# Kernel optimization log

Measured on AMD Instinct MI355X. Metric: run time of the kernel, lower is better.

The kernel has to match this reference:

```python
import jax, jax.numpy as jnp
import numpy as np

K_SIZE = 5


def extract_patches(x, k):
    # tf.image.extract_patches with SAME padding, stride 1, rate 1.
    # x: (B, H, W, C) -> (B, H, W, k*k, C), patch index ordered row-major (ki, kj),
    # channels last within each tap, matching TF's depth ordering + reshape.
    B, H, W, C = x.shape
    p = k // 2
    xp = jnp.pad(x, ((0, 0), (p, p), (p, p), (0, 0)))
    views = [xp[:, i:i + H, j:j + W, :] for i in range(k) for j in range(k)]
    return jnp.stack(views, axis=3)


def setup_inputs() -> dict:
    key = jax.random.key(0)
    k1, k2, k3, k4 = jax.random.split(key, 4)
    B, H, W, C = 4, 64, 64, 128
    bin_size = 128
    return {
        "main": jax.random.normal(k1, (B, H, W, C), dtype=jnp.float32),
        "main_value": jax.random.normal(k2, (B, H, W, bin_size), dtype=jnp.float32),
        "ref": jax.random.normal(k3, (B, H, W, C), dtype=jnp.float32),
        "ref_value": jax.random.normal(k4, (B, H, W, bin_size), dtype=jnp.float32),
    }


def reference(main, main_value, ref, ref_value):
    # mode == 'dot'
    k = K_SIZE
    main5 = main[:, :, :, None, :]                 # (B,H,W,1,C)
    main_value5 = main_value[:, :, :, None, :]     # (B,H,W,1,bin)
    ref_stacked = extract_patches(ref, k)          # (B,H,W,k*k,C)
    ref_value_stacked = extract_patches(ref_value, k)  # (B,H,W,k*k,bin)
    # concat the center query itself as an extra key/value slot
    ref_con = jnp.concatenate([ref_stacked, main5], axis=3)        # (B,H,W,k*k+1,C)
    attn = jnp.sum(ref_con * main5, axis=4)                         # (B,H,W,k*k+1)
    attn = jax.nn.softmax(attn, axis=3)
    val_con = jnp.concatenate([ref_value_stacked, main_value5], axis=3)  # (B,H,W,k*k+1,bin)
    out = jnp.sum(attn[..., None] * val_con, axis=3)                # (B,H,W,bin)
    return out
```

## Files before the change

kernel.cpp:

```cpp
#include <hip/hip_runtime.h>
#include <math.h>

typedef _Float16 v8h __attribute__((ext_vector_type(8)));
typedef float    v4f __attribute__((ext_vector_type(4)));

#define B_OFF   0
#define ALO_OFF 32768
#define L_OFF   40960
#define P_OFF   57344

__device__ __forceinline__ int swz(int r, int c16) {
    return (r << 8) + ((c16 ^ (r & 15)) << 4);
}

__global__ __launch_bounds__(512, 4) void local_attn_mfma(
    const float* __restrict__ main_,
    const float* __restrict__ main_value,
    const float* __restrict__ ref,
    const float* __restrict__ ref_value,
    float* __restrict__ out)
{
    __shared__ __align__(16) char S[65536];

    const int tid = threadIdx.x;
    const int bid = blockIdx.x;
    const int b  = bid >> 7;
    const int h0 = ((bid >> 3) & 15) << 2;
    const int w0 = (bid & 7) << 3;

    {
        const int r = tid >> 2;
        const int q = tid & 3;
        const float* src;
        bool valid = true;
        if (r < 96) {
            const int hy = r / 12, hx = r - hy * 12;
            const int gh = h0 - 2 + hy, gw = w0 - 2 + hx;
            valid = (gh >= 0) & (gh < 64) & (gw >= 0) & (gw < 64);
            src = ref + (size_t)((((b << 6) + (valid ? gh : 0)) << 6) + (valid ? gw : 0)) * 128;
        } else {
            const int t = r - 96;
            src = main_ + (size_t)((((b << 6) + h0 + (t >> 3)) << 6) + (w0 + (t & 7))) * 128;
        }
        #pragma unroll
        for (int g = 0; g < 4; ++g) {
            const int cbase = (q << 5) + (g << 3);
            float a8[8];
            const float4 v0 = valid ? *(const float4*)(src + cbase)     : make_float4(0,0,0,0);
            const float4 v1 = valid ? *(const float4*)(src + cbase + 4) : make_float4(0,0,0,0);
            a8[0]=v0.x; a8[1]=v0.y; a8[2]=v0.z; a8[3]=v0.w;
            a8[4]=v1.x; a8[5]=v1.y; a8[6]=v1.z; a8[7]=v1.w;
            v8h hi;
            #pragma unroll
            for (int j = 0; j < 8; ++j) hi[j] = (_Float16)a8[j];
            *(v8h*)(S + B_OFF + swz(r, (q << 2) + g)) = hi;
            if (r >= 96) {
                v8h lo;
                #pragma unroll
                for (int j = 0; j < 8; ++j) lo[j] = (_Float16)(a8[j] - (float)hi[j]);
                *(v8h*)(S + ALO_OFF + swz(r - 96, (q << 2) + g)) = lo;
            }
        }
        *(uint4*)(S + P_OFF + tid * 16) = make_uint4(0, 0, 0, 0);
    }
    __syncthreads();

    const int lane = tid & 63, w = tid >> 6;
    const int l15 = lane & 15, quad = lane >> 4;
    const int mt  = w >> 2;
    const int ntp = (w & 3) << 1;

    {
        const int arow = 96 + (mt << 4) + l15;
        const int lrow = (mt << 4) + l15;
        const int b0r  = (ntp << 4) + l15, b1r = b0r + 16;
        v4f acc0 = {0,0,0,0}, acc1 = {0,0,0,0};
        #pragma unroll
        for (int ks = 0; ks < 4; ++ks) {
            const int c16 = (ks << 2) + quad;
            const v8h ahi = *(const v8h*)(S + B_OFF   + swz(arow, c16));
            const v8h alo = *(const v8h*)(S + ALO_OFF + swz(lrow, c16));
            const v8h bb0 = *(const v8h*)(S + B_OFF   + swz(b0r,  c16));
            const v8h bb1 = *(const v8h*)(S + B_OFF   + swz(b1r,  c16));
            acc0 = __builtin_amdgcn_mfma_f32_16x16x32_f16(ahi, bb0, acc0, 0, 0, 0);
            acc0 = __builtin_amdgcn_mfma_f32_16x16x32_f16(alo, bb0, acc0, 0, 0, 0);
            acc1 = __builtin_amdgcn_mfma_f32_16x16x32_f16(ahi, bb1, acc1, 0, 0, 0);
            acc1 = __builtin_amdgcn_mfma_f32_16x16x32_f16(alo, bb1, acc1, 0, 0, 0);
        }
        #pragma unroll
        for (int j = 0; j < 4; ++j) {
            const int px = (mt << 4) + (quad << 2) + j;
            *(float*)(S + L_OFF + (px << 9) + ((((ntp    ) << 4) + l15) << 2)) = acc0[j];
            *(float*)(S + L_OFF + (px << 9) + ((((ntp + 1) << 4) + l15) << 2)) = acc1[j];
        }
    }
    __syncthreads();

    {
        #pragma unroll
        for (int i = 0; i < 4; ++i) {
            const int tk = w + (i << 3);
            const int pb = tk & 15;
            const int ch = ((tk >> 4) << 6) + lane;
            v8h hv;
            #pragma unroll
            for (int j = 0; j < 8; ++j) {
                const int pos = (pb << 3) + j;
                float v;
                if (pos < 96) {
                    const int hy = pos / 12, hx = pos - hy * 12;
                    const int gh = h0 - 2 + hy, gw = w0 - 2 + hx;
                    const bool ok = (gh >= 0) & (gh < 64) & (gw >= 0) & (gw < 64);
                    v = ok ? ref_value[(size_t)((((b << 6) + gh) << 6) + gw) * 128 + ch] : 0.f;
                } else {
                    const int t2 = pos - 96;
                    v = main_value[(size_t)((((b << 6) + h0 + (t2 >> 3)) << 6) + (w0 + (t2 & 7))) * 128 + ch];
                }
                hv[j] = (_Float16)v;
            }
            *(v8h*)(S + B_OFF + swz(ch, pb)) = hv;
        }
        #pragma unroll
        for (int i = 0; i < 4; ++i) {
            const int t = (w << 2) + i;
            const int ty = t >> 3, tx = t & 7;
            const bool act = lane < 26;
            int col;
            if (lane < 25) {
                const int dy = lane / 5 - 2, dx = lane % 5 - 2;
                col = (ty + dy + 2) * 12 + (tx + dx + 2);
            } else col = 96 + t;
            const float lg = act ? *(const float*)(S + L_OFF + (t << 9) + (col << 2)) : -INFINITY;
            float m = lg;
            #pragma unroll
            for (int off = 32; off; off >>= 1) m = fmaxf(m, __shfl_xor(m, off));
            const float e = act ? __expf(lg - m) : 0.f;
            float s = e;
            #pragma unroll
            for (int off = 32; off; off >>= 1) s += __shfl_xor(s, off);
            if (act)
                *(_Float16*)(S + P_OFF + swz(t, col >> 3) + ((col & 7) << 1)) = (_Float16)(e / s);
        }
    }
    __syncthreads();

    {
        const int prow = (mt << 4) + l15;
        const int v0r  = (ntp << 4) + l15, v1r = v0r + 16;
        v4f acc0 = {0,0,0,0}, acc1 = {0,0,0,0};
        #pragma unroll
        for (int ks = 0; ks < 4; ++ks) {
            const int c16 = (ks << 2) + quad;
            const v8h pa  = *(const v8h*)(S + P_OFF + swz(prow, c16));
            const v8h vt0 = *(const v8h*)(S + B_OFF + swz(v0r,  c16));
            const v8h vt1 = *(const v8h*)(S + B_OFF + swz(v1r,  c16));
            acc0 = __builtin_amdgcn_mfma_f32_16x16x32_f16(pa, vt0, acc0, 0, 0, 0);
            acc1 = __builtin_amdgcn_mfma_f32_16x16x32_f16(pa, vt1, acc1, 0, 0, 0);
        }
        #pragma unroll
        for (int j = 0; j < 4; ++j) {
            const int px = (mt << 4) + (quad << 2) + j;
            const size_t gbase =
                (size_t)((((b << 6) + h0 + (px >> 3)) << 6) + (w0 + (px & 7))) * 128;
            out[gbase + ((ntp    ) << 4) + l15] = acc0[j];
            out[gbase + ((ntp + 1) << 4) + l15] = acc1[j];
        }
    }
}

extern "C" void kernel_launch(void* const* d_in, const int* in_sizes, int n_in,
                              void* d_out, int out_size, void* d_ws, size_t ws_size,
                              hipStream_t stream) {
    const float* main_      = (const float*)d_in[0];
    const float* main_value = (const float*)d_in[1];
    const float* ref        = (const float*)d_in[2];
    const float* ref_value  = (const float*)d_in[3];
    float* out = (float*)d_out;

    dim3 grid(4 * 16 * 8), block(512);
    local_attn_mfma<<<grid, block, 0, stream>>>(main_, main_value, ref, ref_value, out);
}
```

Before: 99.06 us.

## Prefetch value tiles before first barrier and pack softmax two pixels per wave

```diff
diff --git a/kernel.cpp b/kernel.cpp
--- a/kernel.cpp
+++ b/kernel.cpp
@@ -13,7 +13,7 @@
     return (r << 8) + ((c16 ^ (r & 15)) << 4);
 }
 
-__global__ __launch_bounds__(512, 4) void local_attn_mfma(
+__global__ __launch_bounds__(512, 4) void local_attn_mfma2(
     const float* __restrict__ main_,
     const float* __restrict__ main_value,
     const float* __restrict__ ref,
@@ -27,45 +27,74 @@
     const int b  = bid >> 7;
     const int h0 = ((bid >> 3) & 15) << 2;
     const int w0 = (bid & 7) << 3;
+    const int lane = tid & 63, w = tid >> 6;
 
-    {
-        const int r = tid >> 2;
-        const int q = tid & 3;
-        const float* src;
-        bool valid = true;
-        if (r < 96) {
-            const int hy = r / 12, hx = r - hy * 12;
-            const int gh = h0 - 2 + hy, gw = w0 - 2 + hx;
-            valid = (gh >= 0) & (gh < 64) & (gw >= 0) & (gw < 64);
-            src = ref + (size_t)((((b << 6) + (valid ? gh : 0)) << 6) + (valid ? gw : 0)) * 128;
-        } else {
-            const int t = r - 96;
-            src = main_ + (size_t)((((b << 6) + h0 + (t >> 3)) << 6) + (w0 + (t & 7))) * 128;
+    const int r = tid >> 2;
+    const int q = tid & 3;
+    bool valid = true;
+    const float* src;
+    if (r < 96) {
+        const int hy = r / 12, hx = r - hy * 12;
+        const int gh = h0 - 2 + hy, gw = w0 - 2 + hx;
+        valid = (gh >= 0) & (gh < 64) & (gw >= 0) & (gw < 64);
+        src = ref + (size_t)((((b << 6) + (valid ? gh : 0)) << 6) + (valid ? gw : 0)) * 128;
+    } else {
+        const int t = r - 96;
+        src = main_ + (size_t)((((b << 6) + h0 + (t >> 3)) << 6) + (w0 + (t & 7))) * 128;
+    }
+    float4 e1[8];
+    #pragma unroll
+    for (int g = 0; g < 8; ++g)
+        e1[g] = valid ? *(const float4*)(src + (q << 5) + (g << 2)) : make_float4(0, 0, 0, 0);
+
+    float pv[4][8];
+    #pragma unroll
+    for (int i = 0; i < 4; ++i) {
+        const int tk = w + (i << 3);
+        const int pb = tk & 15;
+        const int ch = ((tk >> 4) << 6) + lane;
+        #pragma unroll
+        for (int j = 0; j < 8; ++j) {
+            const int pos = (pb << 3) + j;
+            float v = 0.f;
+            if (pos < 96) {
+                const int hy = pos / 12, hx = pos - hy * 12;
+                const int gh = h0 - 2 + hy, gw = w0 - 2 + hx;
+                if ((gh >= 0) & (gh < 64) & (gw >= 0) & (gw < 64))
+                    v = ref_value[(size_t)((((b << 6) + gh) << 6) + gw) * 128 + ch];
+            } else {
+                const int t2 = pos - 96;
+                v = main_value[(size_t)((((b << 6) + h0 + (t2 >> 3)) << 6) + (w0 + (t2 & 7))) * 128 + ch];
+            }
+            pv[i][j] = v;
         }
+    }
+
+    #pragma unroll
+    for (int g = 0; g < 4; ++g) {
+        const float4 v0 = e1[2 * g], v1 = e1[2 * g + 1];
+        float a8[8] = {v0.x, v0.y, v0.z, v0.w, v1.x, v1.y, v1.z, v1.w};
+        v8h hi;
         #pragma unroll
-        for (int g = 0; g < 4; ++g) {
-            const int cbase = (q << 5) + (g << 3);
-            float a8[8];
-            const float4 v0 = valid ? *(const float4*)(src + cbase)     : make_float4(0,0,0,0);
-            const float4 v1 = valid ? *(const float4*)(src + cbase + 4) : make_float4(0,0,0,0);
-            a8[0]=v0.x; a8[1]=v0.y; a8[2]=v0.z; a8[3]=v0.w;
-            a8[4]=v1.x; a8[5]=v1.y; a8[6]=v1.z; a8[7]=v1.w;
-            v8h hi;
+        for (int j = 0; j < 8; ++j) hi[j] = (_Float16)a8[j];
+        *(v8h*)(S + B_OFF + swz(r, (q << 2) + g)) = hi;
+        if (r >= 96) {
+            v8h lo;
             #pragma unroll
-            for (int j = 0; j < 8; ++j) hi[j] = (_Float16)a8[j];
-            *(v8h*)(S + B_OFF + swz(r, (q << 2) + g)) = hi;
-            if (r >= 96) {
-                v8h lo;
-                #pragma unroll
-                for (int j = 0; j < 8; ++j) lo[j] = (_Float16)(a8[j] - (float)hi[j]);
-                *(v8h*)(S + ALO_OFF + swz(r - 96, (q << 2) + g)) = lo;
-            }
+            for (int j = 0; j < 8; ++j) lo[j] = (_Float16)(a8[j] - (float)hi[j]);
+            *(v8h*)(S + ALO_OFF + swz(r - 96, (q << 2) + g)) = lo;
         }
-        *(uint4*)(S + P_OFF + tid * 16) = make_uint4(0, 0, 0, 0);
     }
+    *(uint4*)(S + P_OFF + tid * 16) = make_uint4(0, 0, 0, 0);
+
+    v8h hv[4];
+    #pragma unroll
+    for (int i = 0; i < 4; ++i)
+        #pragma unroll
+        for (int j = 0; j < 8; ++j) hv[i][j] = (_Float16)pv[i][j];
+
     __syncthreads();
 
-    const int lane = tid & 63, w = tid >> 6;
     const int l15 = lane & 15, quad = lane >> 4;
     const int mt  = w >> 2;
     const int ntp = (w & 3) << 1;
@@ -74,7 +103,7 @@
         const int arow = 96 + (mt << 4) + l15;
         const int lrow = (mt << 4) + l15;
         const int b0r  = (ntp << 4) + l15, b1r = b0r + 16;
-        v4f acc0 = {0,0,0,0}, acc1 = {0,0,0,0};
+        v4f acc0 = {0, 0, 0, 0}, acc1 = {0, 0, 0, 0};
         #pragma unroll
         for (int ks = 0; ks < 4; ++ks) {
             const int c16 = (ks << 2) + quad;
@@ -102,42 +131,28 @@
             const int tk = w + (i << 3);
             const int pb = tk & 15;
             const int ch = ((tk >> 4) << 6) + lane;
-            v8h hv;
-            #pragma unroll
-            for (int j = 0; j < 8; ++j) {
-                const int pos = (pb << 3) + j;
-                float v;
-                if (pos < 96) {
-                    const int hy = pos / 12, hx = pos - hy * 12;
-                    const int gh = h0 - 2 + hy, gw = w0 - 2 + hx;
-                    const bool ok = (gh >= 0) & (gh < 64) & (gw >= 0) & (gw < 64);
-                    v = ok ? ref_value[(size_t)((((b << 6) + gh) << 6) + gw) * 128 + ch] : 0.f;
-                } else {
-                    const int t2 = pos - 96;
-                    v = main_value[(size_t)((((b << 6) + h0 + (t2 >> 3)) << 6) + (w0 + (t2 & 7))) * 128 + ch];
-                }
-                hv[j] = (_Float16)v;
-            }
-            *(v8h*)(S + B_OFF + swz(ch, pb)) = hv;
+            *(v8h*)(S + B_OFF + swz(ch, pb)) = hv[i];
         }
+        const int half = lane >> 5;
+        const int l    = lane & 31;
         #pragma unroll
-        for (int i = 0; i < 4; ++i) {
-            const int t = (w << 2) + i;
+        for (int i = 0; i < 2; ++i) {
+            const int t = (w << 2) + (i << 1) + half;
             const int ty = t >> 3, tx = t & 7;
-            const bool act = lane < 26;
+            const bool act = l < 26;
             int col;
-            if (lane < 25) {
-                const int dy = lane / 5 - 2, dx = lane % 5 - 2;
+            if (l < 25) {
+                const int dy = l / 5 - 2, dx = l % 5 - 2;
                 col = (ty + dy + 2) * 12 + (tx + dx + 2);
             } else col = 96 + t;
             const float lg = act ? *(const float*)(S + L_OFF + (t << 9) + (col << 2)) : -INFINITY;
             float m = lg;
             #pragma unroll
-            for (int off = 32; off; off >>= 1) m = fmaxf(m, __shfl_xor(m, off));
+            for (int off = 16; off; off >>= 1) m = fmaxf(m, __shfl_xor(m, off));
             const float e = act ? __expf(lg - m) : 0.f;
             float s = e;
             #pragma unroll
-            for (int off = 32; off; off >>= 1) s += __shfl_xor(s, off);
+            for (int off = 16; off; off >>= 1) s += __shfl_xor(s, off);
             if (act)
                 *(_Float16*)(S + P_OFF + swz(t, col >> 3) + ((col & 7) << 1)) = (_Float16)(e / s);
         }
@@ -147,7 +162,7 @@
     {
         const int prow = (mt << 4) + l15;
         const int v0r  = (ntp << 4) + l15, v1r = v0r + 16;
-        v4f acc0 = {0,0,0,0}, acc1 = {0,0,0,0};
+        v4f acc0 = {0, 0, 0, 0}, acc1 = {0, 0, 0, 0};
         #pragma unroll
         for (int ks = 0; ks < 4; ++ks) {
             const int c16 = (ks << 2) + quad;
@@ -178,5 +193,5 @@
     float* out = (float*)d_out;
 
     dim3 grid(4 * 16 * 8), block(512);
-    local_attn_mfma<<<grid, block, 0, stream>>>(main_, main_value, ref, ref_value, out);
+    local_attn_mfma2<<<grid, block, 0, stream>>>(main_, main_value, ref, ref_value, out);
 }
```

Result: no change. 98.64 us (-0.4%).
